# Performance work log

Hardware: AMD Instinct MI355X
Metric: run time of the kernel (lower is better)

The kernel has to match this reference:

```python
import math
import jax, jax.numpy as jnp
import numpy as np

N_NODES = 50_000
N_EDGES = 500_000
INPUT_DIM = 6
HIDDEN = 128
FREQS = 32
LN_EPS = 1e-5
TWO_PI = 2.0 * math.pi


def wrap_angle(a):
    return (a + math.pi) % (2.0 * math.pi) - math.pi


def setup_inputs() -> dict:
    key = jax.random.key(0)
    ks = jax.random.split(key, 12)
    source = jax.random.normal(ks[0], (N_NODES, 5), dtype=jnp.float32)
    target = jax.random.normal(ks[1], (N_NODES, 5), dtype=jnp.float32)
    edge = jax.random.randint(ks[2], (2, N_EDGES), 0, N_NODES, dtype=jnp.int64)
    K = 2 * FREQS + 1
    # FourierEmbedding params: freqs table + 6 per-dim MLPs (Linear->LN->ReLU->Linear), stacked over dim axis
    freqs = jax.random.normal(ks[3], (INPUT_DIM, FREQS), dtype=jnp.float32)
    W1 = jax.random.normal(ks[4], (INPUT_DIM, K, HIDDEN), dtype=jnp.float32) * (1.0 / math.sqrt(K))
    b1 = jnp.zeros((INPUT_DIM, HIDDEN), dtype=jnp.float32)
    ln_w = jnp.ones((INPUT_DIM, HIDDEN), dtype=jnp.float32)
    ln_b = jnp.zeros((INPUT_DIM, HIDDEN), dtype=jnp.float32)
    W2 = jax.random.normal(ks[5], (INPUT_DIM, HIDDEN, HIDDEN), dtype=jnp.float32) * (1.0 / math.sqrt(HIDDEN))
    b2 = jnp.zeros((INPUT_DIM, HIDDEN), dtype=jnp.float32)
    return {"source": source, "target": target, "edge": edge,
            "freqs": freqs, "W1": W1, "b1": b1, "ln_w": ln_w, "ln_b": ln_b,
            "W2": W2, "b2": b2}


def _compute_feature(source, target, edge):
    # source/target: [N, 5] = X, Y, Heading, Speed, (other)
    sp, sh, ss = source[:, :2], source[:, 2], source[:, 3]
    tp, th, ts = target[:, :2], target[:, 2], target[:, 3]
    src, tgt = edge[0], edge[1]
    pd = sp[src] - tp[tgt]                         # [E, 2]
    dx, dy = pd[:, 0], pd[:, 1]
    dist = jnp.sqrt(dx * dx + dy * dy)
    is_close = (dist < 3.0).astype(pd.dtype)
    ang = jnp.arctan2(dy, dx)
    dh = wrap_angle(sh[src] - th[tgt])
    cos_a, sin_a = jnp.cos(ang), jnp.sin(ang)
    tvx, tvy = ts * jnp.cos(th), ts * jnp.sin(th)
    t_close = tvx[tgt] * cos_a + tvy[tgt] * sin_a
    svx, svy = ss * jnp.cos(sh), ss * jnp.sin(sh)
    s_close = svx[src] * cos_a + svy[src] * sin_a
    return jnp.stack([dx, dy, dh, is_close, t_close, s_close], axis=-1)  # [E, 6]


def _fourier_embed(feat, freqs, W1, b1, ln_w, ln_b, W2, b2):
    # feat: [E, 6]; freqs: [6, F]
    x = feat[:, :, None] * freqs[None, :, :] * TWO_PI          # [E, 6, F]
    x = jnp.concatenate([jnp.cos(x), jnp.sin(x), feat[:, :, None]], axis=-1)  # [E, 6, 2F+1]
    h = jnp.einsum('edk,dkh->edh', x, W1) + b1[None]           # [E, 6, H]
    mu = h.mean(axis=-1, keepdims=True)
    var = jnp.mean((h - mu) ** 2, axis=-1, keepdims=True)
    h = (h - mu) * jax.lax.rsqrt(var + LN_EPS) * ln_w[None] + ln_b[None]
    h = jax.nn.relu(h)
    out = jnp.einsum('edh,dhg->edg', h, W2) + b2[None]         # [E, 6, H]
    return out.sum(axis=1)                                     # [E, H]


def reference(source, target, edge, freqs, W1, b1, ln_w, ln_b, W2, b2):
    feat = jax.lax.stop_gradient(_compute_feature(source, target, edge))  # torch.no_grad()
    return _fourier_embed(feat, freqs, W1, b1, ln_w, ln_b, W2, b2)
```

## Files before the change

kernel.cpp:

```cpp
#include <hip/hip_runtime.h>
#include <hip/hip_bf16.h>
#include <math.h>

#define E_EDGES 500000
#define PI_F 3.14159265358979323846f
#define TWOPI_F 6.28318530717958647692f

typedef __attribute__((ext_vector_type(4))) float f32x4;
typedef __attribute__((ext_vector_type(8))) short s16x8;
typedef __attribute__((ext_vector_type(4))) unsigned int u32x4;

static __device__ __forceinline__ short f2bf(float x) {
    __hip_bfloat16 h = __float2bfloat16(x);
    return __builtin_bit_cast(short, h);
}
static __device__ __forceinline__ float bf_lo(unsigned u) {
    return __builtin_bit_cast(float, u << 16);
}
static __device__ __forceinline__ float bf_hi(unsigned u) {
    return __builtin_bit_cast(float, u & 0xFFFF0000u);
}

__global__ void rape_prep_kernel(const float* __restrict__ W1,
                                 const float* __restrict__ W2,
                                 s16x8* __restrict__ ws)
{
    const int d  = blockIdx.x / 24;
    const int sg = blockIdx.x % 24;
    const int j  = threadIdx.x;
    s16x8 v;
    if (sg < 8) {
        const float* W1d = W1 + (size_t)d * 65 * 128;
        const int kb = (sg >> 2) * 32 + (sg & 3) * 4;
        #pragma unroll
        for (int i = 0; i < 4; ++i) {
            v[i]     = f2bf(W1d[(kb + i) * 128 + j]);
            v[i + 4] = f2bf(W1d[(kb + 16 + i) * 128 + j]);
        }
    } else {
        const int sg2 = sg - 8;
        const float* W2d = W2 + (size_t)d * 128 * 128;
        const int kb = (sg2 >> 2) * 32 + (sg2 & 3) * 4;
        #pragma unroll
        for (int i = 0; i < 4; ++i) {
            v[i]     = f2bf(W2d[(kb + i) * 128 + j]);
            v[i + 4] = f2bf(W2d[(kb + 16 + i) * 128 + j]);
        }
    }
    ws[(size_t)d * 24 * 128 + sg * 128 + j] = v;
}

__global__ __launch_bounds__(256, 2)
void rape_mfma11_kernel(const float* __restrict__ source,
                        const float* __restrict__ target,
                        const int*   __restrict__ edge,
                        const float* __restrict__ freqs,
                        const float* __restrict__ W1,
                        const float* __restrict__ b1,
                        const float* __restrict__ ln_w,
                        const float* __restrict__ ln_b,
                        const float* __restrict__ b2,
                        const s16x8* __restrict__ wsg,
                        float* __restrict__ out)
{
    __shared__ s16x8 w1buf[2][8 * 128];
    __shared__ s16x8 w2buf[16 * 128];
    __shared__ float feat_s[6][128];
    __shared__ unsigned b1w_s[768];
    __shared__ unsigned lnwb_s[768];
    __shared__ float freq_s[192];

    const int tid   = threadIdx.x;
    const int lane  = tid & 63;
    const int wv    = tid >> 6;
    const int c     = lane & 15;
    const int g     = lane >> 4;
    const int ebase = blockIdx.x * 128;

    for (int i = tid; i < 768; i += 256) {
        unsigned ub = (unsigned short)f2bf(b1[i]);
        unsigned uw = (unsigned short)f2bf(W1[((size_t)(i >> 7) * 65 + 64) * 128 + (i & 127)]);
        b1w_s[i] = ub | (uw << 16);
        unsigned ulw = (unsigned short)f2bf(ln_w[i]);
        unsigned ulb = (unsigned short)f2bf(ln_b[i]);
        lnwb_s[i] = ulw | (ulb << 16);
    }
    if (tid < 192) freq_s[tid] = freqs[tid];

    if (tid < 128) {
        int ec = ebase + tid; if (ec >= E_EDGES) ec = E_EDGES - 1;
        int si = edge[ec];
        int ti = edge[E_EDGES + ec];
        const float* S = source + (size_t)si * 5;
        const float* T = target + (size_t)ti * 5;
        float spx = S[0], spy = S[1], shd = S[2], ss = S[3];
        float tpx = T[0], tpy = T[1], thd = T[2], ts = T[3];
        float dx = spx - tpx, dy = spy - tpy;
        float dist = sqrtf(dx * dx + dy * dy);
        float ic  = dist < 3.0f ? 1.0f : 0.0f;
        float inv = dist > 0.0f ? 1.0f / dist : 0.0f;
        float ca  = dist > 0.0f ? dx * inv : 1.0f;
        float sa  = dy * inv;
        float a = shd - thd + PI_F;
        float r = fmodf(a, TWOPI_F);
        r = r < 0.0f ? r + TWOPI_F : r;
        float dh = r - PI_F;
        float tc = ts * (cosf(thd) * ca + sinf(thd) * sa);
        float sc = ss * (cosf(shd) * ca + sinf(shd) * sa);
        feat_s[0][tid] = dx; feat_s[1][tid] = dy; feat_s[2][tid] = dh;
        feat_s[3][tid] = ic; feat_s[4][tid] = tc; feat_s[5][tid] = sc;
    }

    {
        const char* gsrc = (const char*)wsg;
        #pragma unroll
        for (int it = 0; it < 4; ++it) {
            const int off = tid * 16 + it * 4096;
            __builtin_amdgcn_global_load_lds(
                (const __attribute__((address_space(1))) unsigned int*)(gsrc + off),
                (__attribute__((address_space(3))) unsigned int*)((char*)w1buf[0] + off),
                16, 0, 0);
        }
    }

    f32x4 acc[2][8];
    #pragma unroll
    for (int gt = 0; gt < 8; ++gt) {
        f32x4 s = {0.f, 0.f, 0.f, 0.f};
        #pragma unroll
        for (int d = 0; d < 6; ++d)
            s += *(const f32x4*)(b2 + d * 128 + gt * 16 + g * 4);
        acc[0][gt] = s; acc[1][gt] = s;
    }

    for (int d = 0; d < 6; ++d) {
        __syncthreads();

        {
            const char* gsrc = (const char*)(wsg + (size_t)d * 24 * 128) + 16384;
            #pragma unroll
            for (int it = 0; it < 8; ++it) {
                const int off = tid * 16 + it * 4096;
                __builtin_amdgcn_global_load_lds(
                    (const __attribute__((address_space(1))) unsigned int*)(gsrc + off),
                    (__attribute__((address_space(3))) unsigned int*)((char*)w2buf + off),
                    16, 0, 0);
            }
        }

        s16x8 bfr[2][2];
        float xv[2];
        const f32x4 fq0 = *(const f32x4*)(freq_s + d * 32 + g * 4);
        const f32x4 fq1 = *(const f32x4*)(freq_s + d * 32 + 16 + g * 4);
        #pragma unroll
        for (int es = 0; es < 2; ++es) {
            const float x = feat_s[d][wv * 32 + es * 16 + c];
            xv[es] = x;
            s16x8 bc, bs;
            #pragma unroll
            for (int i = 0; i < 8; ++i) {
                const float f = (i < 4) ? fq0[i] : fq1[i - 4];
                const float t = x * f;
                const float tf = t - floorf(t);
                bc[i] = f2bf(__builtin_amdgcn_cosf(tf));
                bs[i] = f2bf(__builtin_amdgcn_sinf(tf));
            }
            bfr[es][0] = bc; bfr[es][1] = bs;
        }

        f32x4 d1[2][8];
        #pragma unroll
        for (int jt = 0; jt < 8; ++jt) {
            const u32x4 pw = *(const u32x4*)(b1w_s + d * 128 + jt * 16 + g * 4);
            #pragma unroll
            for (int q = 0; q < 4; ++q) {
                const float bv  = bf_lo(pw[q]);
                const float wv4 = bf_hi(pw[q]);
                d1[0][jt][q] = fmaf(xv[0], wv4, bv);
                d1[1][jt][q] = fmaf(xv[1], wv4, bv);
            }
        }

        __syncthreads();

        #pragma unroll
        for (int jt = 0; jt < 8; ++jt) {
            const s16x8 a0 = w1buf[d & 1][(0 + g) * 128 + jt * 16 + c];
            const s16x8 a1 = w1buf[d & 1][(4 + g) * 128 + jt * 16 + c];
            #pragma unroll
            for (int es = 0; es < 2; ++es) {
                d1[es][jt] = __builtin_amdgcn_mfma_f32_16x16x32_bf16(a0, bfr[es][0], d1[es][jt], 0, 0, 0);
                d1[es][jt] = __builtin_amdgcn_mfma_f32_16x16x32_bf16(a1, bfr[es][1], d1[es][jt], 0, 0, 0);
            }
        }

        if (d < 5) {
            const char* gsrc = (const char*)(wsg + (size_t)(d + 1) * 24 * 128);
            #pragma unroll
            for (int it = 0; it < 4; ++it) {
                const int off = tid * 16 + it * 4096;
                __builtin_amdgcn_global_load_lds(
                    (const __attribute__((address_space(1))) unsigned int*)(gsrc + off),
                    (__attribute__((address_space(3))) unsigned int*)((char*)w1buf[(d + 1) & 1] + off),
                    16, 0, 0);
            }
        }

        float mu[2], rinv[2];
        #pragma unroll
        for (int es = 0; es < 2; ++es) {
            float s1 = 0.f, s2 = 0.f;
            #pragma unroll
            for (int jt = 0; jt < 8; ++jt)
                #pragma unroll
                for (int q = 0; q < 4; ++q) {
                    const float v = d1[es][jt][q];
                    s1 += v; s2 = fmaf(v, v, s2);
                }
            s1 += __shfl_xor(s1, 16); s1 += __shfl_xor(s1, 32);
            s2 += __shfl_xor(s2, 16); s2 += __shfl_xor(s2, 32);
            mu[es] = s1 * 0.0078125f;
            const float var = s2 * 0.0078125f - mu[es] * mu[es];
            rinv[es] = rsqrtf(var + 1e-5f);
        }

        s16x8 pb[2][4];
        #pragma unroll
        for (int ks = 0; ks < 4; ++ks) {
            #pragma unroll
            for (int p = 0; p < 2; ++p) {
                const int jt = 2 * ks + p;
                const u32x4 lnp = *(const u32x4*)(lnwb_s + d * 128 + jt * 16 + g * 4);
                #pragma unroll
                for (int es = 0; es < 2; ++es) {
                    #pragma unroll
                    for (int q = 0; q < 4; ++q) {
                        const float lw = bf_lo(lnp[q]);
                        const float lb = bf_hi(lnp[q]);
                        float hv = (d1[es][jt][q] - mu[es]) * rinv[es];
                        hv = fmaf(hv, lw, lb);
                        hv = fmaxf(hv, 0.f);
                        pb[es][ks][q + 4 * p] = f2bf(hv);
                    }
                }
            }
        }

        #pragma unroll
        for (int ks = 0; ks < 4; ++ks) {
            #pragma unroll
            for (int gt = 0; gt < 8; ++gt) {
                const s16x8 a = w2buf[(ks * 4 + g) * 128 + gt * 16 + c];
                #pragma unroll
                for (int es = 0; es < 2; ++es)
                    acc[es][gt] = __builtin_amdgcn_mfma_f32_16x16x32_bf16(a, pb[es][ks], acc[es][gt], 0, 0, 0);
            }
        }
    }

    #pragma unroll
    for (int es = 0; es < 2; ++es) {
        const int e = ebase + wv * 32 + es * 16 + c;
        if (e < E_EDGES) {
            float* op = out + (size_t)e * 128 + g * 4;
            #pragma unroll
            for (int gt = 0; gt < 8; ++gt)
                *(f32x4*)(op + gt * 16) = acc[es][gt];
        }
    }
}

extern "C" void kernel_launch(void* const* d_in, const int* in_sizes, int n_in,
                              void* d_out, int out_size, void* d_ws, size_t ws_size,
                              hipStream_t stream) {
    const float* source = (const float*)d_in[0];
    const float* target = (const float*)d_in[1];
    const int*   edge   = (const int*)  d_in[2];
    const float* freqs  = (const float*)d_in[3];
    const float* W1     = (const float*)d_in[4];
    const float* b1     = (const float*)d_in[5];
    const float* ln_w   = (const float*)d_in[6];
    const float* ln_b   = (const float*)d_in[7];
    const float* W2     = (const float*)d_in[8];
    const float* b2     = (const float*)d_in[9];
    float* out = (float*)d_out;
    s16x8* wsg = (s16x8*)d_ws;

    rape_prep_kernel<<<6 * 24, 128, 0, stream>>>(W1, W2, wsg);

    const int nblocks = (E_EDGES + 127) / 128;
    rape_mfma11_kernel<<<nblocks, 256, 0, stream>>>(
        source, target, edge, freqs, W1, b1, ln_w, ln_b, b2, wsg, out);
}
```

Baseline: 258.9 us.

## Shrink LDS to a single weight slab and raise occupancy to three blocks

The kernel drops the double-buffered W1 tile and the per-block conversion of b1, ln_w and ln_b. Both the W1 and W2 tiles for each input dim now load into one 48KB slab each iteration. The bias and LayerNorm parameters are packed to bf16 once in the prep kernel and streamed per dim through global_load_lds. The smaller LDS footprint allows launch bounds of 3 blocks per CU, in exchange for losing the prefetch overlap of the next W1 tile behind compute and adding a barrier wait on the full slab load each dim.

```diff
diff --git a/kernel.cpp b/kernel.cpp
--- a/kernel.cpp
+++ b/kernel.cpp
@@ -5,6 +5,7 @@
 #define E_EDGES 500000
 #define PI_F 3.14159265358979323846f
 #define TWOPI_F 6.28318530717958647692f
+#define SLAB_BYTES (6 * 24 * 128 * 16)
 
 typedef __attribute__((ext_vector_type(4))) float f32x4;
 typedef __attribute__((ext_vector_type(8))) short s16x8;
@@ -23,51 +24,61 @@
 
 __global__ void rape_prep_kernel(const float* __restrict__ W1,
                                  const float* __restrict__ W2,
-                                 s16x8* __restrict__ ws)
+                                 const float* __restrict__ b1,
+                                 const float* __restrict__ ln_w,
+                                 const float* __restrict__ ln_b,
+                                 void* __restrict__ wsv)
 {
-    const int d  = blockIdx.x / 24;
-    const int sg = blockIdx.x % 24;
+    const int d  = blockIdx.x / 26;
+    const int sg = blockIdx.x % 26;
     const int j  = threadIdx.x;
-    s16x8 v;
-    if (sg < 8) {
-        const float* W1d = W1 + (size_t)d * 65 * 128;
-        const int kb = (sg >> 2) * 32 + (sg & 3) * 4;
-        #pragma unroll
-        for (int i = 0; i < 4; ++i) {
-            v[i]     = f2bf(W1d[(kb + i) * 128 + j]);
-            v[i + 4] = f2bf(W1d[(kb + 16 + i) * 128 + j]);
-        }
+    if (sg < 24) {
+        s16x8 v;
+        if (sg < 8) {
+            const float* W1d = W1 + (size_t)d * 65 * 128;
+            const int kb = (sg >> 2) * 32 + (sg & 3) * 4;
+            #pragma unroll
+            for (int i = 0; i < 4; ++i) {
+                v[i]     = f2bf(W1d[(kb + i) * 128 + j]);
+                v[i + 4] = f2bf(W1d[(kb + 16 + i) * 128 + j]);
+            }
+        } else {
+            const int sg2 = sg - 8;
+            const float* W2d = W2 + (size_t)d * 128 * 128;
+            const int kb = (sg2 >> 2) * 32 + (sg2 & 3) * 4;
+            #pragma unroll
+            for (int i = 0; i < 4; ++i) {
+                v[i]     = f2bf(W2d[(kb + i) * 128 + j]);
+                v[i + 4] = f2bf(W2d[(kb + 16 + i) * 128 + j]);
+            }
+        }
+        ((s16x8*)wsv)[(size_t)d * 24 * 128 + sg * 128 + j] = v;
     } else {
-        const int sg2 = sg - 8;
-        const float* W2d = W2 + (size_t)d * 128 * 128;
-        const int kb = (sg2 >> 2) * 32 + (sg2 & 3) * 4;
-        #pragma unroll
-        for (int i = 0; i < 4; ++i) {
-            v[i]     = f2bf(W2d[(kb + i) * 128 + j]);
-            v[i + 4] = f2bf(W2d[(kb + 16 + i) * 128 + j]);
-        }
-    }
-    ws[(size_t)d * 24 * 128 + sg * 128 + j] = v;
-}
-
-__global__ __launch_bounds__(256, 2)
-void rape_mfma11_kernel(const float* __restrict__ source,
+        unsigned* prm = (unsigned*)((char*)wsv + SLAB_BYTES) + d * 256 + (sg - 24) * 128 + j;
+        unsigned lo, hi;
+        if (sg == 24) {
+            lo = (unsigned short)f2bf(b1[d * 128 + j]);
+            hi = (unsigned short)f2bf(W1[((size_t)d * 65 + 64) * 128 + j]);
+        } else {
+            lo = (unsigned short)f2bf(ln_w[d * 128 + j]);
+            hi = (unsigned short)f2bf(ln_b[d * 128 + j]);
+        }
+        *prm = lo | (hi << 16);
+    }
+}
+
+__global__ __launch_bounds__(256, 3)
+void rape_mfma12_kernel(const float* __restrict__ source,
                         const float* __restrict__ target,
                         const int*   __restrict__ edge,
                         const float* __restrict__ freqs,
-                        const float* __restrict__ W1,
-                        const float* __restrict__ b1,
-                        const float* __restrict__ ln_w,
-                        const float* __restrict__ ln_b,
                         const float* __restrict__ b2,
-                        const s16x8* __restrict__ wsg,
+                        const void*  __restrict__ wsg,
                         float* __restrict__ out)
 {
-    __shared__ s16x8 w1buf[2][8 * 128];
-    __shared__ s16x8 w2buf[16 * 128];
+    __shared__ s16x8 slab[24 * 128];
+    __shared__ unsigned prm_s[256];
     __shared__ float feat_s[6][128];
-    __shared__ unsigned b1w_s[768];
-    __shared__ unsigned lnwb_s[768];
     __shared__ float freq_s[192];
 
     const int tid   = threadIdx.x;
@@ -77,14 +88,6 @@
     const int g     = lane >> 4;
     const int ebase = blockIdx.x * 128;
 
-    for (int i = tid; i < 768; i += 256) {
-        unsigned ub = (unsigned short)f2bf(b1[i]);
-        unsigned uw = (unsigned short)f2bf(W1[((size_t)(i >> 7) * 65 + 64) * 128 + (i & 127)]);
-        b1w_s[i] = ub | (uw << 16);
-        unsigned ulw = (unsigned short)f2bf(ln_w[i]);
-        unsigned ulb = (unsigned short)f2bf(ln_b[i]);
-        lnwb_s[i] = ulw | (ulb << 16);
-    }
     if (tid < 192) freq_s[tid] = freqs[tid];
 
     if (tid < 128) {
@@ -111,18 +114,6 @@
         feat_s[3][tid] = ic; feat_s[4][tid] = tc; feat_s[5][tid] = sc;
     }
 
-    {
-        const char* gsrc = (const char*)wsg;
-        #pragma unroll
-        for (int it = 0; it < 4; ++it) {
-            const int off = tid * 16 + it * 4096;
-            __builtin_amdgcn_global_load_lds(
-                (const __attribute__((address_space(1))) unsigned int*)(gsrc + off),
-                (__attribute__((address_space(3))) unsigned int*)((char*)w1buf[0] + off),
-                16, 0, 0);
-        }
-    }
-
     f32x4 acc[2][8];
     #pragma unroll
     for (int gt = 0; gt < 8; ++gt) {
@@ -137,13 +128,20 @@
         __syncthreads();
 
         {
-            const char* gsrc = (const char*)(wsg + (size_t)d * 24 * 128) + 16384;
-            #pragma unroll
-            for (int it = 0; it < 8; ++it) {
+            const char* gsrc = (const char*)wsg + (size_t)d * 24 * 128 * 16;
+            #pragma unroll
+            for (int it = 0; it < 12; ++it) {
                 const int off = tid * 16 + it * 4096;
                 __builtin_amdgcn_global_load_lds(
                     (const __attribute__((address_space(1))) unsigned int*)(gsrc + off),
-                    (__attribute__((address_space(3))) unsigned int*)((char*)w2buf + off),
+                    (__attribute__((address_space(3))) unsigned int*)((char*)slab + off),
+                    16, 0, 0);
+            }
+            if (tid < 64) {
+                const char* psrc = (const char*)wsg + SLAB_BYTES + d * 1024 + tid * 16;
+                __builtin_amdgcn_global_load_lds(
+                    (const __attribute__((address_space(1))) unsigned int*)psrc,
+                    (__attribute__((address_space(3))) unsigned int*)((char*)prm_s + tid * 16),
                     16, 0, 0);
             }
         }
@@ -168,10 +166,12 @@
             bfr[es][0] = bc; bfr[es][1] = bs;
         }
 
+        __syncthreads();
+
         f32x4 d1[2][8];
         #pragma unroll
         for (int jt = 0; jt < 8; ++jt) {
-            const u32x4 pw = *(const u32x4*)(b1w_s + d * 128 + jt * 16 + g * 4);
+            const u32x4 pw = *(const u32x4*)(prm_s + jt * 16 + g * 4);
             #pragma unroll
             for (int q = 0; q < 4; ++q) {
                 const float bv  = bf_lo(pw[q]);
@@ -181,28 +181,14 @@
             }
         }
 
-        __syncthreads();
-
         #pragma unroll
         for (int jt = 0; jt < 8; ++jt) {
-            const s16x8 a0 = w1buf[d & 1][(0 + g) * 128 + jt * 16 + c];
-            const s16x8 a1 = w1buf[d & 1][(4 + g) * 128 + jt * 16 + c];
+            const s16x8 a0 = slab[(0 + g) * 128 + jt * 16 + c];
+            const s16x8 a1 = slab[(4 + g) * 128 + jt * 16 + c];
             #pragma unroll
             for (int es = 0; es < 2; ++es) {
                 d1[es][jt] = __builtin_amdgcn_mfma_f32_16x16x32_bf16(a0, bfr[es][0], d1[es][jt], 0, 0, 0);
                 d1[es][jt] = __builtin_amdgcn_mfma_f32_16x16x32_bf16(a1, bfr[es][1], d1[es][jt], 0, 0, 0);
-            }
-        }
-
-        if (d < 5) {
-            const char* gsrc = (const char*)(wsg + (size_t)(d + 1) * 24 * 128);
-            #pragma unroll
-            for (int it = 0; it < 4; ++it) {
-                const int off = tid * 16 + it * 4096;
-                __builtin_amdgcn_global_load_lds(
-                    (const __attribute__((address_space(1))) unsigned int*)(gsrc + off),
-                    (__attribute__((address_space(3))) unsigned int*)((char*)w1buf[(d + 1) & 1] + off),
-                    16, 0, 0);
             }
         }
 
@@ -230,7 +216,7 @@
             #pragma unroll
             for (int p = 0; p < 2; ++p) {
                 const int jt = 2 * ks + p;
-                const u32x4 lnp = *(const u32x4*)(lnwb_s + d * 128 + jt * 16 + g * 4);
+                const u32x4 lnp = *(const u32x4*)(prm_s + 128 + jt * 16 + g * 4);
                 #pragma unroll
                 for (int es = 0; es < 2; ++es) {
                     #pragma unroll
@@ -250,7 +236,7 @@
         for (int ks = 0; ks < 4; ++ks) {
             #pragma unroll
             for (int gt = 0; gt < 8; ++gt) {
-                const s16x8 a = w2buf[(ks * 4 + g) * 128 + gt * 16 + c];
+                const s16x8 a = slab[(8 + ks * 4 + g) * 128 + gt * 16 + c];
                 #pragma unroll
                 for (int es = 0; es < 2; ++es)
                     acc[es][gt] = __builtin_amdgcn_mfma_f32_16x16x32_bf16(a, pb[es][ks], acc[es][gt], 0, 0, 0);
@@ -284,11 +270,11 @@
     const float* W2     = (const float*)d_in[8];
     const float* b2     = (const float*)d_in[9];
     float* out = (float*)d_out;
-    s16x8* wsg = (s16x8*)d_ws;
-
-    rape_prep_kernel<<<6 * 24, 128, 0, stream>>>(W1, W2, wsg);
+    void* wsg = d_ws;
+
+    rape_prep_kernel<<<6 * 26, 128, 0, stream>>>(W1, W2, b1, ln_w, ln_b, wsg);
 
     const int nblocks = (E_EDGES + 127) / 128;
-    rape_mfma11_kernel<<<nblocks, 256, 0, stream>>>(
-        source, target, edge, freqs, W1, b1, ln_w, ln_b, b2, wsg, out);
-}
+    rape_mfma12_kernel<<<nblocks, 256, 0, stream>>>(
+        source, target, edge, freqs, b2, wsg, out);
+}
```

Result: slower. 290.1 us (+12.1%).
